# Optimization experiments

Measured on AMD Instinct MI355X. Metric: run time of the kernel, lower is better.

The kernel has to match this reference:

```python
import jax, jax.numpy as jnp
import numpy as np

DILATIONS = [1, 2, 4, 8, 16, 32, 64, 128, 256, 512] * 2
WD = 128   # residual/gate channels
SD = 512   # skip channels
VOCAB = 256
FIELD = int(np.sum(DILATIONS)) + 2  # receptive field = 2048


def setup_inputs() -> dict:
    key = jax.random.key(0)
    ks = jax.random.split(key, 10)
    B, T = 4, 16384
    L = len(DILATIONS)
    y = jax.random.randint(ks[0], (B, T), 0, VOCAB)
    embed = jax.random.normal(ks[1], (VOCAB, WD), dtype=jnp.float32) * 0.1
    # dilated causal conv: kernel_size=2, wd -> 2*wd (gate stacking)
    Wd = jax.random.normal(ks[2], (L, 2 * WD, WD, 2), dtype=jnp.float32) * 0.05
    bd = jnp.zeros((L, 2 * WD), dtype=jnp.float32)
    # skip 1x1 conv: wd -> sd
    Ws = jax.random.normal(ks[3], (L, SD, WD, 1), dtype=jnp.float32) * 0.05
    bs = jnp.zeros((L, SD), dtype=jnp.float32)
    # residual 1x1 conv: wd -> wd
    Wr = jax.random.normal(ks[4], (L, WD, WD, 1), dtype=jnp.float32) * 0.05
    br = jnp.zeros((L, WD), dtype=jnp.float32)
    # post convs (bias=False)
    W1 = jax.random.normal(ks[5], (SD, SD, 1), dtype=jnp.float32) * 0.05
    W2 = jax.random.normal(ks[6], (VOCAB, SD, 1), dtype=jnp.float32) * 0.05
    return {"y": y, "embed": embed, "Wd": Wd, "bd": bd, "Ws": Ws,
            "bs": bs, "Wr": Wr, "br": br, "W1": W1, "W2": W2}


def reference(y, embed, Wd, bd, Ws, bs, Wr, br, W1, W2):
    # embedding -> [B, C, T]
    x = jnp.transpose(embed[y], (0, 2, 1))
    finalout = x.shape[2] - (FIELD - 1)
    skip = None
    for i, d in enumerate(DILATIONS):
        # dilated valid conv with kernel size 2 == two shifted 1x1 matmuls
        in_act = (jnp.einsum('oc,bct->bot', Wd[i, :, :, 0], x[:, :, :-d]) +
                  jnp.einsum('oc,bct->bot', Wd[i, :, :, 1], x[:, :, d:]) +
                  bd[i][None, :, None])                       # [B, 2*WD, T-d]
        acts = jnp.tanh(in_act[:, :WD]) * jax.nn.sigmoid(in_act[:, WD:])
        res = jnp.einsum('oc,bct->bot', Wr[i, :, :, 0], acts) + br[i][None, :, None]
        sk = (jnp.einsum('oc,bct->bot', Ws[i, :, :, 0], acts[:, :, -finalout:]) +
              bs[i][None, :, None])                            # [B, SD, finalout]
        skip = sk if skip is None else skip + sk
        x = res + x[:, :, d:]
    out = jax.nn.relu(skip)
    out = jax.nn.relu(jnp.einsum('oc,bct->bot', W1[:, :, 0], out))
    out = jnp.einsum('oc,bct->bot', W2[:, :, 0], out)          # [B, 256, finalout]
    return out
```

## Files before the change

kernel.cpp:

```cpp
#include <hip/hip_runtime.h>
#include <cstddef>

#define B_    4
#define T_    16384
#define FOUT_ 14337
#define FOUTP 14464
#define NL_   20
#define XSTR  ((size_t)T_*128)
#define ABSTR ((size_t)FOUTP*128)
#define ALSTR ((size_t)B_*FOUTP*128)
#define SBSTR ((size_t)FOUTP*512)

typedef float    f32x16 __attribute__((ext_vector_type(16)));
typedef _Float16 f16x8  __attribute__((ext_vector_type(8)));

__device__ _Float16 g_xh0[(size_t)B_*T_*128];
__device__ _Float16 g_xh1[(size_t)B_*T_*128];
__device__ _Float16 g_WdF0[(size_t)NL_*256*128];
__device__ _Float16 g_WdF1[(size_t)NL_*256*128];
__device__ _Float16 g_WrF [(size_t)NL_*128*128];
__device__ _Float16 g_WsF [(size_t)512*2560];
__device__ _Float16 g_W1F [(size_t)512*512];
__device__ _Float16 g_W2F [(size_t)256*512];
__device__ float    g_bssum[512];
__device__ _Float16 g_acts[(size_t)NL_*B_*FOUTP*128];
__device__ _Float16 g_skipF[(size_t)B_*FOUTP*512];
__device__ _Float16 g_h1F [(size_t)B_*FOUTP*512];

__device__ __forceinline__ float sigm_(float x){ return 1.0f/(1.0f+__expf(-x)); }
__device__ __forceinline__ float tanh_(float x){ return 1.0f - 2.0f/(__expf(2.0f*x)+1.0f); }
__device__ __forceinline__ f32x16 MFMA32(f16x8 a, f16x8 b, f32x16 c){
  return __builtin_amdgcn_mfma_f32_32x32x16_f16(a, b, c, 0, 0, 0);
}

typedef const __attribute__((address_space(1))) _Float16 gash;
typedef __attribute__((address_space(3))) _Float16 lash;
__device__ __forceinline__ void gld_lds16(const _Float16* g, _Float16* l){
  __builtin_amdgcn_global_load_lds((gash*)g, (lash*)l, 16, 0, 0);
}

__global__ void cvt_wd(const float* __restrict__ Wd){
  int i = blockIdx.x*256 + threadIdx.x;
  if (i >= NL_*256*16) return;
  int row = i >> 4, koct = i & 15;
  const float* s = Wd + ((size_t)row*128 + koct*8)*2;
  int lane = (koct&1)*32 + (row&31);
  size_t addr = (size_t)((row>>5)*8 + (koct>>1))*512 + lane*8;
  union { _Float16 h[8]; uint4 v; } u0, u1;
#pragma unroll
  for (int j=0;j<8;j++){ u0.h[j]=(_Float16)s[2*j]; u1.h[j]=(_Float16)s[2*j+1]; }
  *(uint4*)((void*)(g_WdF0 + addr)) = u0.v;
  *(uint4*)((void*)(g_WdF1 + addr)) = u1.v;
}
__global__ void cvt_rm(const float* __restrict__ src, int which, int M, int K){
  int i = blockIdx.x*256 + threadIdx.x;
  if (i >= M*(K>>3)) return;
  int row = i / (K>>3), koct = i % (K>>3);
  const float* s = src + (size_t)row*K + koct*8;
  int lane = (koct&1)*32 + (row&31);
  size_t addr = ((size_t)(row>>5)*(K>>4) + (koct>>1))*512 + lane*8;
  union { _Float16 h[8]; uint4 v; } u;
#pragma unroll
  for (int j=0;j<8;j++) u.h[j]=(_Float16)s[j];
  _Float16* dst = (which==0)?g_WrF:(which==1)?g_W1F:g_W2F;
  *(uint4*)((void*)(dst + addr)) = u.v;
}
__global__ void cvt_ws(const float* __restrict__ Ws){
  int i = blockIdx.x*256 + threadIdx.x;
  if (i >= NL_*512*16) return;
  int l = i >> 13, o = (i>>4)&511, coct = i&15;
  const float* s = Ws + ((size_t)(l*512+o))*128 + coct*8;
  int lane = (coct&1)*32 + (o&31);
  size_t addr = ((size_t)(o>>5)*160 + (size_t)(l*8 + (coct>>1)))*512 + lane*8;
  union { _Float16 h[8]; uint4 v; } u;
#pragma unroll
  for (int j=0;j<8;j++) u.h[j]=(_Float16)s[j];
  *(uint4*)((void*)(g_WsF + addr)) = u.v;
}
__global__ void bssum_k(const float* __restrict__ bs){
  int o = threadIdx.x;
  float s = 0.f;
  for (int l=0;l<NL_;l++) s += bs[l*512 + o];
  g_bssum[o] = s;
}

__global__ void embed_kernel(const int* __restrict__ y, const float* __restrict__ embed){
  int gid = blockIdx.x*256 + threadIdx.x;
  int bt = gid >> 4, c8 = gid & 15;
  if (bt < B_*T_){
    int idx = y[bt];
    const float* e = embed + (size_t)idx*128 + c8*8;
    union { _Float16 h[8]; uint4 v; } u;
#pragma unroll
    for (int j=0;j<8;j++) u.h[j]=(_Float16)e[j];
    *(uint4*)((void*)(g_xh0 + (size_t)bt*128 + c8*8)) = u.v;
  }
}

__global__ __launch_bounds__(256,3) void layer16(
    int swap, int l, int d, int Tout, int ss,
    const float* __restrict__ bd_l, const float* __restrict__ br_l)
{
  const _Float16* __restrict__ xin  = swap ? g_xh1 : g_xh0;
  _Float16* __restrict__       xout = swap ? g_xh0 : g_xh1;

  __shared__ _Float16 X0s[16*520];
  __shared__ _Float16 X1s[16*520];
  __shared__ _Float16 ACs[16*520];

  const int tid = threadIdx.x;
  const int w   = tid >> 6;
  const int lane= tid & 63;
  const int ln2 = lane & 31;
  const int h   = lane >> 5;
  const int b   = blockIdx.y;
  const int t0  = blockIdx.x*64;
  const int ntv = min(64, Tout - t0);
  const int limit = Tout + d - 1;
  const _Float16* __restrict__ xb = xin + (size_t)b*XSTR;

#pragma unroll
  for (int it=0; it<4; it++){
    int t = (tid>>4) + it*16, c16 = tid&15;
    int s0 = t0 + t;     if (s0 > limit) s0 = limit;
    int s1 = t0 + t + d; if (s1 > limit) s1 = limit;
    *(uint4*)((void*)&X0s[c16*520 + t*8]) = *(const uint4*)((const void*)(xb + (size_t)s0*128 + c16*8));
    *(uint4*)((void*)&X1s[c16*520 + t*8]) = *(const uint4*)((const void*)(xb + (size_t)s1*128 + c16*8));
  }
  __syncthreads();

  f32x16 aB[2][2];
#pragma unroll
  for (int mi=0;mi<2;mi++)
#pragma unroll
    for (int nt=0;nt<2;nt++)
#pragma unroll
      for (int r=0;r<16;r++) aB[mi][nt][r] = 0.f;

#pragma unroll
  for (int tap=0; tap<2; tap++){
    const _Float16* __restrict__ Xs = tap ? X1s : X0s;
    const _Float16* __restrict__ Wt = (tap ? g_WdF1 : g_WdF0) + (size_t)l*32768;
    const _Float16* aT = Wt + (size_t)w*4096 + lane*8;
    const _Float16* aS = Wt + (size_t)(4+w)*4096 + lane*8;
#pragma unroll
    for (int ks=0; ks<8; ks++){
      f16x8 bfr[2];
#pragma unroll
      for (int nt=0; nt<2; nt++)
        bfr[nt] = *(const f16x8*)((const void*)&Xs[(ks*2+h)*520 + (nt*32+ln2)*8]);
      f16x8 fT = *(const f16x8*)((const void*)(aT + ks*512));
      f16x8 fS = *(const f16x8*)((const void*)(aS + ks*512));
#pragma unroll
      for (int nt=0; nt<2; nt++){
        aB[0][nt] = MFMA32(fT, bfr[nt], aB[0][nt]);
        aB[1][nt] = MFMA32(fS, bfr[nt], aB[1][nt]);
      }
    }
  }

#pragma unroll
  for (int nt=0; nt<2; nt++)
#pragma unroll
    for (int rq=0; rq<4; rq++){
      int c0 = w*32 + rq*8 + 4*h;
      union { _Float16 hh[4]; ushort4 v; } pk;
#pragma unroll
      for (int rr=0; rr<4; rr++){
        float it_ = aB[0][nt][rq*4+rr] + bd_l[c0+rr];
        float is_ = aB[1][nt][rq*4+rr] + bd_l[128+c0+rr];
        pk.hh[rr] = (_Float16)(tanh_(it_)*sigm_(is_));
      }
      *(ushort4*)((void*)&ACs[(w*4+rq)*520 + (nt*32+ln2)*8 + 4*h]) = pk.v;
    }
  __syncthreads();

  f32x16 aC[2];
#pragma unroll
  for (int nt=0;nt<2;nt++)
#pragma unroll
    for (int r=0;r<16;r++) aC[nt][r] = 0.f;
  {
    const _Float16* aW = g_WrF + (size_t)l*16384 + (size_t)w*4096 + lane*8;
#pragma unroll
    for (int ks=0; ks<8; ks++){
      f16x8 bfr[2];
#pragma unroll
      for (int nt=0; nt<2; nt++)
        bfr[nt] = *(const f16x8*)((const void*)&ACs[(ks*2+h)*520 + (nt*32+ln2)*8]);
      f16x8 fW = *(const f16x8*)((const void*)(aW + ks*512));
#pragma unroll
      for (int nt=0; nt<2; nt++)
        aC[nt] = MFMA32(fW, bfr[nt], aC[nt]);
    }
  }

#pragma unroll
  for (int nt=0; nt<2; nt++){
    int t = nt*32 + ln2;
    if (t < ntv){
      size_t xrow = (size_t)b*XSTR + (size_t)(t0+t)*128;
#pragma unroll
      for (int rq=0; rq<4; rq++){
        int c0 = w*32 + rq*8 + 4*h;
        union { ushort4 v; _Float16 hh[4]; } xr;
        xr.v = *(const ushort4*)((const void*)&X1s[(w*4+rq)*520 + t*8 + 4*h]);
        union { _Float16 hh[4]; ushort4 v; } ov;
#pragma unroll
        for (int rr=0; rr<4; rr++)
          ov.hh[rr] = (_Float16)(aC[nt][rq*4+rr] + br_l[c0+rr] + (float)xr.hh[rr]);
        *(ushort4*)((void*)(xout + xrow + c0)) = ov.v;
      }
    }
  }

  _Float16* __restrict__ actsB = g_acts + (size_t)l*ALSTR + (size_t)b*ABSTR;
#pragma unroll
  for (int it=0; it<4; it++){
    int t = (tid>>4) + it*16, c16 = tid&15;
    int ts = t0 + t - ss;
    if (t < ntv && ts >= 0 && ts < FOUT_){
      size_t addr = (size_t)(ts>>5)*4096 + (size_t)(c16>>1)*512 + ((c16&1)*32 + (ts&31))*8;
      *(uint4*)((void*)(actsB + addr)) = *(const uint4*)((const void*)&ACs[c16*520 + t*8]);
    }
  }
}

template<int MODE>
__global__ __launch_bounds__(512,4) void gemm_stream(float* __restrict__ outF){
  constexpr int NSTEP = (MODE==0)?160:32;
  constexpr int NSC   = NSTEP/4;
  const _Float16* __restrict__ A    = (MODE==0)?g_WsF:(MODE==1)?g_W1F:g_W2F;
  const _Float16* __restrict__ Bsrc = (MODE==0)?g_acts:(MODE==1)?g_skipF:g_h1F;

  __shared__ __align__(16) _Float16 Bs[4][8192];

  const int tid = threadIdx.x;
  const int w   = tid >> 6;
  const int lane= tid & 63;
  const int ln2 = lane & 31;
  const int h   = lane >> 5;
  const int b   = blockIdx.z;
  const int ts0 = blockIdx.y*128;
  const int mtile = blockIdx.x*8 + w;

  const _Float16* Gq[2];
#pragma unroll
  for (int q=0;q<2;q++){
    int nt = (w*2+q)&3;
    size_t tile = (size_t)blockIdx.y*4 + nt;
    Gq[q] = (MODE==0) ? (Bsrc + (size_t)b*ABSTR + tile*4096  + lane*8)
                      : (Bsrc + (size_t)b*SBSTR + tile*16384 + lane*8);
  }

  const _Float16* Aw = A + (size_t)mtile*((size_t)NSTEP*512) + lane*8;

  f32x16 acc[4];
#pragma unroll
  for (int nt=0;nt<4;nt++)
#pragma unroll
    for (int r=0;r<16;r++) acc[nt][r] = 0.f;

  auto STAGE = [&](int buf, int sc){
#pragma unroll
    for (int q=0;q<2;q++){
      int bi   = w*2 + q;
      int kslq = bi>>2;
      const _Float16* g;
      if (MODE==0){
        int ks = sc*4 + kslq;
        g = Gq[q] + (size_t)(ks>>3)*ALSTR + (size_t)(ks&7)*512;
      } else {
        g = Gq[q] + (size_t)(sc*4 + kslq)*512;
      }
      gld_lds16(g, &Bs[buf][(size_t)bi*512]);
    }
  };

  STAGE(0,0);
  STAGE(1,1);
  asm volatile("s_waitcnt vmcnt(2)" ::: "memory");
  __builtin_amdgcn_sched_barrier(0);
  __builtin_amdgcn_s_barrier();

  for (int c=0; c<NSC; ++c){
    const int buf = c & 3;
    f16x8 af[4];
#pragma unroll
    for (int j=0;j<4;j++)
      af[j] = *(const f16x8*)((const void*)(Aw + (size_t)(c*4+j)*512));
    __builtin_amdgcn_sched_barrier(0);
    if (c+2 < NSC) STAGE((c+2)&3, c+2);
    __builtin_amdgcn_sched_barrier(0);
#pragma unroll
    for (int j=0;j<4;j++){
      f16x8 bfr[4];
#pragma unroll
      for (int nt=0;nt<4;nt++)
        bfr[nt] = *(const f16x8*)((const void*)&Bs[buf][(size_t)(j*4+nt)*512 + lane*8]);
#pragma unroll
      for (int nt=0;nt<4;nt++)
        acc[nt] = MFMA32(af[j], bfr[nt], acc[nt]);
    }
    __builtin_amdgcn_sched_barrier(0);
    __builtin_amdgcn_s_barrier();
  }

  if (MODE != 2){
    _Float16* __restrict__ dstb = ((MODE==0)?g_skipF:g_h1F) + (size_t)b*SBSTR;
#pragma unroll
    for (int nt=0; nt<4; nt++){
      int ts = ts0 + nt*32 + ln2;
      if (ts >= FOUT_) continue;
#pragma unroll
      for (int rq=0; rq<4; rq++){
        int m0 = mtile*32 + rq*8 + 4*h;
        union { _Float16 hh[4]; ushort4 v; } pk;
#pragma unroll
        for (int rr=0; rr<4; rr++){
          float vv = acc[nt][rq*4+rr];
          if (MODE==0) vv += g_bssum[m0+rr];
          pk.hh[rr] = (_Float16)fmaxf(vv, 0.f);
        }
        size_t addr = (size_t)(ts>>5)*16384 + (size_t)(mtile*2 + (rq>>1))*512
                    + ((rq&1)*32 + (ts&31))*8 + 4*h;
        *(ushort4*)((void*)(dstb + addr)) = pk.v;
      }
    }
  } else {
#pragma unroll
    for (int nt=0; nt<4; nt++){
      int ts = ts0 + nt*32 + ln2;
      if (ts >= FOUT_) continue;
#pragma unroll
      for (int rq=0; rq<4; rq++){
        int m0 = w*32 + rq*8 + 4*h;
#pragma unroll
        for (int rr=0; rr<4; rr++)
          outF[((size_t)(b*256 + m0 + rr))*FOUT_ + ts] = acc[nt][rq*4+rr];
      }
    }
  }
}

extern "C" void kernel_launch(void* const* d_in, const int* in_sizes, int n_in,
                              void* d_out, int out_size, void* d_ws, size_t ws_size,
                              hipStream_t stream) {
  const int*   y     = (const int*)  d_in[0];
  const float* embed = (const float*)d_in[1];
  const float* Wd    = (const float*)d_in[2];
  const float* bd    = (const float*)d_in[3];
  const float* Ws    = (const float*)d_in[4];
  const float* bs    = (const float*)d_in[5];
  const float* Wr    = (const float*)d_in[6];
  const float* br    = (const float*)d_in[7];
  const float* W1    = (const float*)d_in[8];
  const float* W2    = (const float*)d_in[9];
  float* out = (float*)d_out;
  (void)d_ws; (void)ws_size;

  cvt_wd<<<dim3(320), dim3(256), 0, stream>>>(Wd);
  cvt_rm<<<dim3(160), dim3(256), 0, stream>>>(Wr, 0, NL_*128, 128);
  cvt_rm<<<dim3(128), dim3(256), 0, stream>>>(W1, 1, 512, 512);
  cvt_rm<<<dim3( 64), dim3(256), 0, stream>>>(W2, 2, 256, 512);
  cvt_ws<<<dim3(640), dim3(256), 0, stream>>>(Ws);
  bssum_k<<<dim3(1), dim3(512), 0, stream>>>(bs);

  embed_kernel<<<dim3((B_*T_*16)/256), dim3(256), 0, stream>>>(y, embed);

  static const int DIL[NL_] = {1,2,4,8,16,32,64,128,256,512,
                               1,2,4,8,16,32,64,128,256,512};
  int swap = 0;
  int Tin = T_;
  for (int i=0;i<NL_;i++){
    int d = DIL[i];
    int Tout = Tin - d;
    dim3 grid((Tout+63)/64, B_);
    layer16<<<grid, dim3(256), 0, stream>>>(
        swap, i, d, Tout, Tout - FOUT_, bd + (size_t)i*256, br + (size_t)i*128);
    swap ^= 1;
    Tin = Tout;
  }

  gemm_stream<0><<<dim3(2, FOUTP/128, B_), dim3(512), 0, stream>>>(nullptr);
  gemm_stream<1><<<dim3(2, FOUTP/128, B_), dim3(512), 0, stream>>>(nullptr);
  gemm_stream<2><<<dim3(1, FOUTP/128, B_), dim3(512), 0, stream>>>(out);
}
```

Baseline: 958.9 us.

## Widen layer tile to 128 timesteps with 8 waves, swizzled LDS, reuse X0 buffer

```diff
diff --git a/kernel.cpp b/kernel.cpp
--- a/kernel.cpp
+++ b/kernel.cpp
@@ -97,35 +97,39 @@
   }
 }
 
-__global__ __launch_bounds__(256,3) void layer16(
+__device__ __forceinline__ int xh_(int r, int t){ return r*1024 + ((t ^ (r&7))*8); }
+
+__global__ __launch_bounds__(512,4) void layer16(
     int swap, int l, int d, int Tout, int ss,
     const float* __restrict__ bd_l, const float* __restrict__ br_l)
 {
   const _Float16* __restrict__ xin  = swap ? g_xh1 : g_xh0;
   _Float16* __restrict__       xout = swap ? g_xh0 : g_xh1;
 
-  __shared__ _Float16 X0s[16*520];
-  __shared__ _Float16 X1s[16*520];
-  __shared__ _Float16 ACs[16*520];
+  __shared__ _Float16 X0s[16*1024];
+  __shared__ _Float16 X1s[16*1024];
+  _Float16* ACs = X0s;
 
   const int tid = threadIdx.x;
   const int w   = tid >> 6;
   const int lane= tid & 63;
   const int ln2 = lane & 31;
   const int h   = lane >> 5;
+  const int wm  = w & 3;
+  const int wn  = w >> 2;
   const int b   = blockIdx.y;
-  const int t0  = blockIdx.x*64;
-  const int ntv = min(64, Tout - t0);
+  const int t0  = blockIdx.x*128;
+  const int ntv = min(128, Tout - t0);
   const int limit = Tout + d - 1;
   const _Float16* __restrict__ xb = xin + (size_t)b*XSTR;
 
 #pragma unroll
   for (int it=0; it<4; it++){
-    int t = (tid>>4) + it*16, c16 = tid&15;
+    int t = (tid>>4) + it*32, c16 = tid&15;
     int s0 = t0 + t;     if (s0 > limit) s0 = limit;
     int s1 = t0 + t + d; if (s1 > limit) s1 = limit;
-    *(uint4*)((void*)&X0s[c16*520 + t*8]) = *(const uint4*)((const void*)(xb + (size_t)s0*128 + c16*8));
-    *(uint4*)((void*)&X1s[c16*520 + t*8]) = *(const uint4*)((const void*)(xb + (size_t)s1*128 + c16*8));
+    *(uint4*)((void*)&X0s[xh_(c16,t)]) = *(const uint4*)((const void*)(xb + (size_t)s0*128 + c16*8));
+    *(uint4*)((void*)&X1s[xh_(c16,t)]) = *(const uint4*)((const void*)(xb + (size_t)s1*128 + c16*8));
   }
   __syncthreads();
 
@@ -141,14 +145,14 @@
   for (int tap=0; tap<2; tap++){
     const _Float16* __restrict__ Xs = tap ? X1s : X0s;
     const _Float16* __restrict__ Wt = (tap ? g_WdF1 : g_WdF0) + (size_t)l*32768;
-    const _Float16* aT = Wt + (size_t)w*4096 + lane*8;
-    const _Float16* aS = Wt + (size_t)(4+w)*4096 + lane*8;
+    const _Float16* aT = Wt + (size_t)wm*4096 + lane*8;
+    const _Float16* aS = Wt + (size_t)(4+wm)*4096 + lane*8;
 #pragma unroll
     for (int ks=0; ks<8; ks++){
       f16x8 bfr[2];
 #pragma unroll
       for (int nt=0; nt<2; nt++)
-        bfr[nt] = *(const f16x8*)((const void*)&Xs[(ks*2+h)*520 + (nt*32+ln2)*8]);
+        bfr[nt] = *(const f16x8*)((const void*)&Xs[xh_(ks*2+h, (wn*2+nt)*32+ln2)]);
       f16x8 fT = *(const f16x8*)((const void*)(aT + ks*512));
       f16x8 fS = *(const f16x8*)((const void*)(aS + ks*512));
 #pragma unroll
@@ -158,12 +162,13 @@
       }
     }
   }
+  __syncthreads();
 
 #pragma unroll
   for (int nt=0; nt<2; nt++)
 #pragma unroll
     for (int rq=0; rq<4; rq++){
-      int c0 = w*32 + rq*8 + 4*h;
+      int c0 = wm*32 + rq*8 + 4*h;
       union { _Float16 hh[4]; ushort4 v; } pk;
 #pragma unroll
       for (int rr=0; rr<4; rr++){
@@ -171,7 +176,7 @@
         float is_ = aB[1][nt][rq*4+rr] + bd_l[128+c0+rr];
         pk.hh[rr] = (_Float16)(tanh_(it_)*sigm_(is_));
       }
-      *(ushort4*)((void*)&ACs[(w*4+rq)*520 + (nt*32+ln2)*8 + 4*h]) = pk.v;
+      *(ushort4*)((void*)&ACs[xh_(wm*4+rq, (wn*2+nt)*32+ln2) + 4*h]) = pk.v;
     }
   __syncthreads();
 
@@ -181,13 +186,13 @@
 #pragma unroll
     for (int r=0;r<16;r++) aC[nt][r] = 0.f;
   {
-    const _Float16* aW = g_WrF + (size_t)l*16384 + (size_t)w*4096 + lane*8;
+    const _Float16* aW = g_WrF + (size_t)l*16384 + (size_t)wm*4096 + lane*8;
 #pragma unroll
     for (int ks=0; ks<8; ks++){
       f16x8 bfr[2];
 #pragma unroll
       for (int nt=0; nt<2; nt++)
-        bfr[nt] = *(const f16x8*)((const void*)&ACs[(ks*2+h)*520 + (nt*32+ln2)*8]);
+        bfr[nt] = *(const f16x8*)((const void*)&ACs[xh_(ks*2+h, (wn*2+nt)*32+ln2)]);
       f16x8 fW = *(const f16x8*)((const void*)(aW + ks*512));
 #pragma unroll
       for (int nt=0; nt<2; nt++)
@@ -197,14 +202,14 @@
 
 #pragma unroll
   for (int nt=0; nt<2; nt++){
-    int t = nt*32 + ln2;
+    int t = (wn*2+nt)*32 + ln2;
     if (t < ntv){
       size_t xrow = (size_t)b*XSTR + (size_t)(t0+t)*128;
 #pragma unroll
       for (int rq=0; rq<4; rq++){
-        int c0 = w*32 + rq*8 + 4*h;
+        int c0 = wm*32 + rq*8 + 4*h;
         union { ushort4 v; _Float16 hh[4]; } xr;
-        xr.v = *(const ushort4*)((const void*)&X1s[(w*4+rq)*520 + t*8 + 4*h]);
+        xr.v = *(const ushort4*)((const void*)&X1s[xh_(wm*4+rq, t) + 4*h]);
         union { _Float16 hh[4]; ushort4 v; } ov;
 #pragma unroll
         for (int rr=0; rr<4; rr++)
@@ -217,11 +222,11 @@
   _Float16* __restrict__ actsB = g_acts + (size_t)l*ALSTR + (size_t)b*ABSTR;
 #pragma unroll
   for (int it=0; it<4; it++){
-    int t = (tid>>4) + it*16, c16 = tid&15;
+    int t = (tid>>4) + it*32, c16 = tid&15;
     int ts = t0 + t - ss;
     if (t < ntv && ts >= 0 && ts < FOUT_){
       size_t addr = (size_t)(ts>>5)*4096 + (size_t)(c16>>1)*512 + ((c16&1)*32 + (ts&31))*8;
-      *(uint4*)((void*)(actsB + addr)) = *(const uint4*)((const void*)&ACs[c16*520 + t*8]);
+      *(uint4*)((void*)(actsB + addr)) = *(const uint4*)((const void*)&ACs[xh_(c16,t)]);
     }
   }
 }
@@ -375,8 +380,8 @@
   for (int i=0;i<NL_;i++){
     int d = DIL[i];
     int Tout = Tin - d;
-    dim3 grid((Tout+63)/64, B_);
-    layer16<<<grid, dim3(256), 0, stream>>>(
+    dim3 grid((Tout+127)/128, B_);
+    layer16<<<grid, dim3(512), 0, stream>>>(
         swap, i, d, Tout, Tout - FOUT_, bd + (size_t)i*256, br + (size_t)i*128);
     swap ^= 1;
     Tin = Tout;
```

New measurement: 1.001 ms. 1.04x slower.
